# Performance work log

Hardware: AMD Instinct MI355X
Metric: run time of the kernel (lower is better)

Reference implementation:

```python
import jax, jax.numpy as jnp
import numpy as np

N, E, G = 50000, 400000, 500
H, C, IN, ED = 4, 64, 9, 3
NEG = 0.2   # LeakyReLU negative slope (PyG GATv2 default)
EPS = 1e-5  # BatchNorm eps


def _gatv2(x, src, dst, ea, Wl, bl, Wr, We, att, bias):
    # PyG GATv2Conv, concat=False (mean over heads), eval mode (no dropout)
    xl = (x @ Wl + bl).reshape(-1, H, C)   # source transform  [N,H,C]
    xr = (x @ Wr).reshape(-1, H, C)        # target transform  [N,H,C]
    ee = (ea @ We).reshape(-1, H, C)       # edge transform    [E,H,C]
    m = xl[src] + xr[dst] + ee             # [E,H,C]
    s = jnp.einsum('ehc,hc->eh', jax.nn.leaky_relu(m, NEG), att)  # [E,H]
    smax = jax.ops.segment_max(s, dst, num_segments=N)
    ex = jnp.exp(s - smax[dst])
    den = jax.ops.segment_sum(ex, dst, num_segments=N)
    alpha = ex / den[dst]                  # segment softmax over in-edges of dst
    out = jax.ops.segment_sum(xl[src] * alpha[:, :, None], dst, num_segments=N)
    return out.mean(axis=1) + bias         # [N,C]


def _bn(x, g, b, mu, var):
    return (x - mu) * (g * jax.lax.rsqrt(var + EPS)) + b


def setup_inputs() -> dict:
    key = jax.random.key(0)
    ks = jax.random.split(key, 32)
    f = lambda k, s: (jax.random.normal(k, s, jnp.float32) * 0.1)
    inp = dict(
        x=jax.random.normal(ks[0], (N, IN), jnp.float32),
        edge_index=jax.random.randint(ks[1], (2, E), 0, N),
        batch=jnp.sort(jax.random.randint(ks[2], (N,), 0, G)),
        edge_attr=jax.random.normal(ks[3], (E, ED), jnp.float32),
        # input head conv (in=9)
        W0l=f(ks[4], (IN, H * C)), b0l=f(ks[5], (H * C,)),
        W0r=f(ks[6], (IN, H * C)), W0e=f(ks[7], (ED, H * C)),
        a0=f(ks[8], (H, C)), c0=f(ks[9], (C,)),
        # 3 residual conv layers (in=64), stacked
        Wl=f(ks[10], (3, C, H * C)), bl=f(ks[11], (3, H * C)),
        Wr=f(ks[12], (3, C, H * C)), We=f(ks[13], (3, ED, H * C)),
        a=f(ks[14], (3, H, C)), cb=f(ks[15], (3, C)),
        # 4 batchnorms (eval mode running stats)
        bn_g=jnp.ones((4, C), jnp.float32) + f(ks[16], (4, C)),
        bn_b=f(ks[17], (4, C)),
        bn_m=f(ks[18], (4, C)),
        bn_v=jnp.ones((4, C), jnp.float32),
        # output MLP head
        Wo1=f(ks[19], (C, C // 2)), bo1=f(ks[20], (C // 2,)),
        Wo2=f(ks[21], (C // 2, 1)), bo2=f(ks[22], (1,)),
    )
    return inp


def reference(x, edge_index, batch, edge_attr,
              W0l, b0l, W0r, W0e, a0, c0,
              Wl, bl, Wr, We, a, cb,
              bn_g, bn_b, bn_m, bn_v,
              Wo1, bo1, Wo2, bo2):
    src, dst = edge_index[0], edge_index[1]
    h = _gatv2(x, src, dst, edge_attr, W0l, b0l, W0r, W0e, a0, c0)
    h = jax.nn.elu(_bn(h, bn_g[0], bn_b[0], bn_m[0], bn_v[0]))
    for i in range(3):
        z = _gatv2(h, src, dst, edge_attr, Wl[i], bl[i], Wr[i], We[i], a[i], cb[i])
        z = jax.nn.elu(_bn(z, bn_g[i + 1], bn_b[i + 1], bn_m[i + 1], bn_v[i + 1]))
        h = h + z
    # global mean pool over graphs
    cnt = jax.ops.segment_sum(jnp.ones((N,), h.dtype), batch, num_segments=G)
    pooled = jax.ops.segment_sum(h, batch, num_segments=G) / jnp.maximum(cnt, 1.0)[:, None]
    hid = jax.nn.elu(pooled @ Wo1 + bo1)
    return hid @ Wo2 + bo2  # [G,1]
```

## Files before the change

### kernel.cpp

```cpp
#include <hip/hip_runtime.h>
#include <hip/hip_fp16.h>
#include <math.h>

typedef _Float16 h2 __attribute__((ext_vector_type(2)));
typedef _Float16 h8 __attribute__((ext_vector_type(8)));
typedef float f4 __attribute__((ext_vector_type(4)));

#define NWAVES 8192

static __device__ __forceinline__ h2 u2h2(unsigned u) {
    union { unsigned u; h2 h; } x; x.u = u; return x.h;
}

__global__ __launch_bounds__(256) void count_kernel(const int* __restrict__ dst,
                                                    int* __restrict__ deg, int E) {
    int e = blockIdx.x * 256 + threadIdx.x;
    if (e < E) atomicAdd(&deg[dst[e]], 1);
}

#define SCAN_TPB 256
#define SCAN_VPT 4
#define SCAN_ELEMS (SCAN_TPB * SCAN_VPT)

__global__ __launch_bounds__(256) void scan_phase1(const int* __restrict__ deg,
                                                   int* __restrict__ bsum, int n) {
    __shared__ int sh[SCAN_TPB];
    int base = blockIdx.x * SCAN_ELEMS + threadIdx.x * SCAN_VPT;
    int s = 0;
#pragma unroll
    for (int j = 0; j < SCAN_VPT; j++) { int i = base + j; if (i < n) s += deg[i]; }
    sh[threadIdx.x] = s;
    __syncthreads();
    for (int off = 128; off; off >>= 1) {
        if (threadIdx.x < (unsigned)off) sh[threadIdx.x] += sh[threadIdx.x + off];
        __syncthreads();
    }
    if (threadIdx.x == 0) bsum[blockIdx.x] = sh[0];
}

__global__ __launch_bounds__(256) void scan_phase2(int* __restrict__ bsum, int nb,
                                                   int* __restrict__ rowptr, int n) {
    __shared__ int sh[256];
    int v = (threadIdx.x < (unsigned)nb) ? bsum[threadIdx.x] : 0;
    sh[threadIdx.x] = v;
    __syncthreads();
    for (int off = 1; off < 256; off <<= 1) {
        int t = (threadIdx.x >= (unsigned)off) ? sh[threadIdx.x - off] : 0;
        __syncthreads();
        sh[threadIdx.x] += t;
        __syncthreads();
    }
    if (threadIdx.x < (unsigned)nb) bsum[threadIdx.x] = sh[threadIdx.x] - v;
    if (threadIdx.x == 0) rowptr[n] = sh[255];
}

__global__ __launch_bounds__(256) void scan_phase3(const int* __restrict__ deg,
                                                   const int* __restrict__ bsum,
                                                   int* __restrict__ rowptr,
                                                   int* __restrict__ cursor, int n) {
    __shared__ int sh[SCAN_TPB];
    int tid = threadIdx.x;
    int base = blockIdx.x * SCAN_ELEMS + tid * SCAN_VPT;
    int v[SCAN_VPT];
    int s = 0;
#pragma unroll
    for (int j = 0; j < SCAN_VPT; j++) { int i = base + j; v[j] = (i < n) ? deg[i] : 0; s += v[j]; }
    sh[tid] = s;
    __syncthreads();
    for (int off = 1; off < SCAN_TPB; off <<= 1) {
        int t = (tid >= off) ? sh[tid - off] : 0;
        __syncthreads();
        sh[tid] += t;
        __syncthreads();
    }
    int ex = sh[tid] - s + bsum[blockIdx.x];
#pragma unroll
    for (int j = 0; j < SCAN_VPT; j++) {
        int i = base + j;
        if (i < n) { rowptr[i] = ex; cursor[i] = ex; ex += v[j]; }
    }
}

__global__ __launch_bounds__(256) void scatter_kernel(const int* __restrict__ src,
                                                      const int* __restrict__ dst,
                                                      const float* __restrict__ ea,
                                                      int* __restrict__ cursor,
                                                      uint4* __restrict__ csr4, int E) {
    int e = blockIdx.x * 256 + threadIdx.x;
    if (e < E) {
        int d = dst[e];
        int pos = atomicAdd(&cursor[d], 1);
        size_t eb3 = (size_t)e * 3;
        uint4 r;
        r.x = (unsigned)src[e];
        __half2 p0, p1, p2;
        p0.x = p0.y = __float2half_rn(ea[eb3]);
        p1.x = p1.y = __float2half_rn(ea[eb3 + 1]);
        p2.x = p2.y = __float2half_rn(ea[eb3 + 2]);
        r.y = *(unsigned*)&p0; r.z = *(unsigned*)&p1; r.w = *(unsigned*)&p2;
        csr4[pos] = r;
    }
}

__global__ __launch_bounds__(256) void wbal_kernel(const int* __restrict__ rowptr,
                                                   int Nn, int* __restrict__ wstart) {
    int q = blockIdx.x * 256 + threadIdx.x;
    if (q > NWAVES) return;
    if (q == 0) { wstart[0] = 0; return; }
    if (q == NWAVES) { wstart[NWAVES] = Nn; return; }
    int Etot = rowptr[Nn];
    int t = (int)(((long long)q * Etot) / NWAVES);
    int lo = 0, hi = Nn;
    while (lo < hi) {
        int mid = (lo + hi) >> 1;
        if (rowptr[mid] < t) lo = mid + 1; else hi = mid;
    }
    wstart[q] = lo;
}

__global__ __launch_bounds__(256) void bnprep_kernel(const float* __restrict__ c0,
                                                     const float* __restrict__ cb,
                                                     const float* __restrict__ bng,
                                                     const float* __restrict__ bnb,
                                                     const float* __restrict__ bnm,
                                                     const float* __restrict__ bnv,
                                                     float* __restrict__ epi) {
    int t = threadIdx.x;
    int l = t >> 6, c = t & 63;
    float s = bng[l * 64 + c] * rsqrtf(bnv[l * 64 + c] + 1e-5f);
    float bias = (l == 0) ? c0[c] : cb[(l - 1) * 64 + c];
    epi[l * 128 + c] = 0.25f * s;
    epi[l * 128 + 64 + c] = (bias - bnm[l * 64 + c]) * s + bnb[l * 64 + c];
}

__global__ __launch_bounds__(256) void gstart_kernel(const int* __restrict__ batch,
                                                     int* __restrict__ gstart,
                                                     int Nn, int Gg) {
    int n = blockIdx.x * 256 + threadIdx.x;
    if (n >= Nn) return;
    int b = batch[n];
    int prev = (n == 0) ? -1 : batch[n - 1];
    for (int g = prev + 1; g <= b; g++) gstart[g] = n;
    if (n == Nn - 1)
        for (int g = b + 1; g <= Gg; g++) gstart[g] = Nn;
}

__global__ __launch_bounds__(256) void wprep_kernel(const float* __restrict__ W0l,
                                                    const float* __restrict__ W0r,
                                                    const float* __restrict__ Wl,
                                                    const float* __restrict__ Wr,
                                                    __half* __restrict__ Wp) {
    int t = blockIdx.x * 256 + threadIdx.x;
    int layer = t >> 12;
    int r = t & 4095;
    int lane = r & 63;
    int ks = (r >> 6) & 1;
    int gct = r >> 7;
    int K = (layer == 0) ? 9 : 64;
    const float* Wsrc;
    if (layer == 0) Wsrc = (gct < 16) ? W0l : W0r;
    else            Wsrc = ((gct < 16) ? Wl : Wr) + (size_t)(layer - 1) * 64 * 256;
    int cl = ((gct & 15) << 4) + (lane & 15);
    int k0 = (ks << 5) + ((lane >> 4) << 3);
    __half vals[8] __attribute__((aligned(16)));
#pragma unroll
    for (int j = 0; j < 8; j++) {
        int k = k0 + j;
        vals[j] = __float2half_rn((k < K) ? Wsrc[(size_t)k * 256 + cl] : 0.f);
    }
    *(uint4*)(Wp + (size_t)t * 8) = *(const uint4*)vals;
}

template <int K>
__global__ __launch_bounds__(256) void gemm2_mfma_kernel(const float* __restrict__ xin,
                                                         const __half* __restrict__ Wp,
                                                         const float* __restrict__ bl,
                                                         __half* __restrict__ xl,
                                                         __half* __restrict__ xr, int Nn) {
    constexpr int NKS = (K > 32) ? 2 : 1;
    constexpr int KP = NKS * 32;
    __shared__ __align__(16) float shx[32][KP + 4];
    int tid = threadIdx.x;
    int lane = tid & 63;
    int wv = tid >> 6;
    int nb = blockIdx.x * 32;
    int l15 = lane & 15;
    int lg = lane >> 4;

    if (K != KP) {
        for (int q = tid; q < 32 * KP; q += 256) shx[q / KP][q % KP] = 0.f;
        __syncthreads();
    }
    if (K == 64) {
        for (int q = tid; q < 32 * 16; q += 256) {
            int r = q >> 4, c4 = q & 15;
            int node = nb + r;
            float4 v = (node < Nn) ? *(const float4*)(xin + (size_t)node * 64 + c4 * 4)
                                   : make_float4(0.f, 0.f, 0.f, 0.f);
            *(float4*)&shx[r][c4 * 4] = v;
        }
    } else {
        for (int q = tid; q < 32 * K; q += 256) {
            int r = q / K, c = q - r * K;
            int node = nb + r;
            shx[r][c] = (node < Nn) ? xin[(size_t)node * K + c] : 0.f;
        }
    }
    __syncthreads();

    h8 afr[8][NKS];
#pragma unroll
    for (int i = 0; i < 8; i++) {
        int gct = wv * 8 + i;
#pragma unroll
        for (int ks = 0; ks < NKS; ks++)
            afr[i][ks] = *(const h8*)(Wp + (((size_t)(gct * 2 + ks)) * 64 + lane) * 8);
    }
    h8 bfr[2][NKS];
#pragma unroll
    for (int nt = 0; nt < 2; nt++) {
        int row = nt * 16 + l15;
#pragma unroll
        for (int ks = 0; ks < NKS; ks++) {
            int k0 = ks * 32 + lg * 8;
            float4 f0 = *(const float4*)&shx[row][k0];
            float4 f1 = *(const float4*)&shx[row][k0 + 4];
            h8 b;
            b[0] = (_Float16)f0.x; b[1] = (_Float16)f0.y;
            b[2] = (_Float16)f0.z; b[3] = (_Float16)f0.w;
            b[4] = (_Float16)f1.x; b[5] = (_Float16)f1.y;
            b[6] = (_Float16)f1.z; b[7] = (_Float16)f1.w;
            bfr[nt][ks] = b;
        }
    }
    f4 acc[8][2];
#pragma unroll
    for (int i = 0; i < 8; i++) {
        int gct = wv * 8 + i;
        f4 ini;
        if (gct < 16) {
            float4 b4 = *(const float4*)(bl + (gct << 4) + (lg << 2));
            ini[0] = b4.x; ini[1] = b4.y; ini[2] = b4.z; ini[3] = b4.w;
        } else {
            ini[0] = 0.f; ini[1] = 0.f; ini[2] = 0.f; ini[3] = 0.f;
        }
        acc[i][0] = ini;
        acc[i][1] = ini;
    }
#pragma unroll
    for (int i = 0; i < 8; i++)
#pragma unroll
        for (int nt = 0; nt < 2; nt++)
#pragma unroll
            for (int ks = 0; ks < NKS; ks++)
                acc[i][nt] = __builtin_amdgcn_mfma_f32_16x16x32_f16(
                    afr[i][ks], bfr[nt][ks], acc[i][nt], 0, 0, 0);
#pragma unroll
    for (int i = 0; i < 8; i++) {
        int gct = wv * 8 + i;
        __half* outp = (gct < 16) ? xl : xr;
        int cl = ((gct & 15) << 4) + (lg << 2);
#pragma unroll
        for (int nt = 0; nt < 2; nt++) {
            int node = nb + nt * 16 + l15;
            if (node < Nn) {
                __half h4[4] __attribute__((aligned(8)));
                h4[0] = __float2half_rn(acc[i][nt][0]);
                h4[1] = __float2half_rn(acc[i][nt][1]);
                h4[2] = __float2half_rn(acc[i][nt][2]);
                h4[3] = __float2half_rn(acc[i][nt][3]);
                *(uint2*)(outp + (size_t)node * 256 + cl) = *(const uint2*)h4;
            }
        }
    }
}

#define EB 6

#define GISSUE(S, ibase)                                                               \
    {                                                                                  \
        _Pragma("unroll") for (int j = 0; j < EB; j++) {                               \
            int idx = (ibase) + j;                                                     \
            if (idx < end) {                                                           \
                uint4 ce = csr4[idx];                   \
                cey##S[j] = ce.y; cez##S[j] = ce.z; cew##S[j] = ce.w;                  \
                int sn = (int)ce.x;                                                    \
                xpk##S[j] = *(const uint2*)(xl + ((size_t)sn << 8) + (lane << 2));     \
            } else {                                                                   \
                cey##S[j] = 0u; cez##S[j] = 0u; cew##S[j] = 0u;                        \
                xpk##S[j] = make_uint2(0u, 0u);                                        \
            }                                                                          \
        }                                                                              \
    }

#define GCOMPUTE(S, ibase)                                                             \
    {                                                                                  \
        float p[EB];                                                                   \
        _Pragma("unroll") for (int j = 0; j < EB; j++) {                               \
            int idx = (ibase) + j;                                                     \
            if (idx < end) {                                                           \
                h2 ea0 = u2h2(cey##S[j]);                                              \
                h2 ea1 = u2h2(cez##S[j]);                                              \
                h2 ea2 = u2h2(cew##S[j]);                                              \
                h2 xl01 = u2h2(xpk##S[j].x);                                           \
                h2 xl23 = u2h2(xpk##S[j].y);                                           \
                h2 t01 = __builtin_elementwise_fma(ea0, we0a,                          \
                           __builtin_elementwise_fma(ea1, we1a,                        \
                             __builtin_elementwise_fma(ea2, we2a, xr01))) + xl01;      \
                h2 t23 = __builtin_elementwise_fma(ea0, we0b,                          \
                           __builtin_elementwise_fma(ea1, we1b,                        \
                             __builtin_elementwise_fma(ea2, we2b, xr23))) + xl23;      \
                h2 l01 = __builtin_elementwise_max(t01, t01 * c02);                    \
                h2 l23 = __builtin_elementwise_max(t23, t23 * c02);                    \
                p[j] = __builtin_amdgcn_fdot2(l01, atta,                               \
                           __builtin_amdgcn_fdot2(l23, attb, 0.f, false), false);      \
            } else p[j] = -INFINITY;                                                   \
        }                                                                              \
        _Pragma("unroll") for (int off = 1; off < 16; off <<= 1) {                     \
            _Pragma("unroll") for (int j = 0; j < EB; j++) p[j] += __shfl_xor(p[j], off); \
        }                                                                              \
        _Pragma("unroll") for (int j = 0; j < EB; j++) {                               \
            float wv2 = __expf(p[j]);                                                  \
            float2 f0 = __half22float2(*(const __half2*)&xpk##S[j].x);                 \
            float2 f1 = __half22float2(*(const __half2*)&xpk##S[j].y);                 \
            f4 xf; xf[0] = f0.x; xf[1] = f0.y; xf[2] = f1.x; xf[3] = f1.y;             \
            acc = acc + wv2 * xf;                                                      \
            l_run += wv2;                                                              \
        }                                                                              \
    }

__global__ __launch_bounds__(256) void gat_kernel(const __half* __restrict__ xl,
                                                  const __half* __restrict__ xr,
                                                  const float* __restrict__ We,
                                                  const float* __restrict__ att,
                                                  const float* __restrict__ epi,
                                                  const int* __restrict__ rowptr,
                                                  const int* __restrict__ wstart,
                                                  const uint4* __restrict__ csr4,
                                                  float* __restrict__ hout,
                                                  const float* __restrict__ hres,
                                                  int Nn) {
    int tid = threadIdx.x;
    int lane = tid & 63;
    int w = __builtin_amdgcn_readfirstlane(tid >> 6);
    int wave = blockIdx.x * 4 + w;

    float4 we0f = *(const float4*)&We[lane * 4];
    float4 we1f = *(const float4*)&We[256 + lane * 4];
    float4 we2f = *(const float4*)&We[512 + lane * 4];
    float4 attf = *(const float4*)&att[lane * 4];
    h2 we0a = { (_Float16)we0f.x, (_Float16)we0f.y };
    h2 we0b = { (_Float16)we0f.z, (_Float16)we0f.w };
    h2 we1a = { (_Float16)we1f.x, (_Float16)we1f.y };
    h2 we1b = { (_Float16)we1f.z, (_Float16)we1f.w };
    h2 we2a = { (_Float16)we2f.x, (_Float16)we2f.y };
    h2 we2b = { (_Float16)we2f.z, (_Float16)we2f.w };
    h2 atta = { (_Float16)attf.x, (_Float16)attf.y };
    h2 attb = { (_Float16)attf.z, (_Float16)attf.w };
    h2 c02 = { (_Float16)0.2f, (_Float16)0.2f };
    float4 eA = *(const float4*)&epi[(lane & 15) * 4];
    float4 eB4 = *(const float4*)&epi[64 + (lane & 15) * 4];

    int ns = wstart[wave], ne = wstart[wave + 1];
    int d = ns;
    if (d >= ne) return;
    int beg = rowptr[d];
    int end = rowptr[d + 1];
    uint2 xrp = *(const uint2*)(xr + ((size_t)d << 8) + (lane << 2));

    uint2 xpkA[EB], xpkB[EB];
    unsigned ceyA[EB], cezA[EB], cewA[EB], ceyB[EB], cezB[EB], cewB[EB];

    while (d < ne) {
        int dn = d + 1;
        int begn = 0, endn = 0;
        uint2 xrpn = make_uint2(0u, 0u);
        if (dn < ne) {
            begn = rowptr[dn];
            endn = rowptr[dn + 1];
            xrpn = *(const uint2*)(xr + ((size_t)dn << 8) + (lane << 2));
        }
        h2 xr01 = u2h2(xrp.x);
        h2 xr23 = u2h2(xrp.y);

        float l_run = 0.f;
        f4 acc; acc[0] = 0.f; acc[1] = 0.f; acc[2] = 0.f; acc[3] = 0.f;

        int i = beg;
        if (i < end) {
            GISSUE(A, i);
            for (;;) {
                int nx = i + EB;
                if (nx < end) GISSUE(B, nx);
                GCOMPUTE(A, i);
                i = nx;
                if (i >= end) break;
                nx = i + EB;
                if (nx < end) GISSUE(A, nx);
                GCOMPUTE(B, i);
                i = nx;
                if (i >= end) break;
            }
        }
        float inv = (end > beg) ? 1.f / l_run : 0.f;
        float4 o = make_float4(acc[0] * inv, acc[1] * inv, acc[2] * inv, acc[3] * inv);
#pragma unroll
        for (int off = 16; off < 64; off <<= 1) {
            o.x += __shfl_xor(o.x, off);
            o.y += __shfl_xor(o.y, off);
            o.z += __shfl_xor(o.z, off);
            o.w += __shfl_xor(o.w, off);
        }
        if (lane < 16) {
            float vx = fmaf(o.x, eA.x, eB4.x);
            float vy = fmaf(o.y, eA.y, eB4.y);
            float vz = fmaf(o.z, eA.z, eB4.z);
            float vw = fmaf(o.w, eA.w, eB4.w);
            vx = vx > 0.f ? vx : expm1f(vx);
            vy = vy > 0.f ? vy : expm1f(vy);
            vz = vz > 0.f ? vz : expm1f(vz);
            vw = vw > 0.f ? vw : expm1f(vw);
            if (hres) {
                float4 r4 = *(const float4*)&hres[((size_t)d << 6) + (lane << 2)];
                vx += r4.x; vy += r4.y; vz += r4.z; vw += r4.w;
            }
            *(float4*)&hout[((size_t)d << 6) + (lane << 2)] = make_float4(vx, vy, vz, vw);
        }
        d = dn; beg = begn; end = endn; xrp = xrpn;
    }
}

__global__ __launch_bounds__(256) void pool_kernel(const float* __restrict__ h,
                                                   const int* __restrict__ gstart,
                                                   float* __restrict__ pooled, int Gg) {
    __shared__ float red[4][64];
    int g = blockIdx.x;
    int tid = threadIdx.x;
    int lane = tid & 63, w = tid >> 6;
    int gs = gstart[g], ge = gstart[g + 1];
    float s = 0.f;
    for (int n = gs + w; n < ge; n += 4) s += h[((size_t)n << 6) + lane];
    red[w][lane] = s;
    __syncthreads();
    if (tid < 64) {
        float tot = red[0][tid] + red[1][tid] + red[2][tid] + red[3][tid];
        float c = fmaxf((float)(ge - gs), 1.f);
        pooled[((size_t)g << 6) + tid] = tot / c;
    }
}

__global__ __launch_bounds__(64) void head_kernel(const float* __restrict__ pooled,
                                                  const float* __restrict__ Wo1,
                                                  const float* __restrict__ bo1,
                                                  const float* __restrict__ Wo2,
                                                  const float* __restrict__ bo2,
                                                  float* __restrict__ out, int Gg) {
    int g = blockIdx.x;
    int t = threadIdx.x;
    __shared__ float sp[64];
    sp[t] = pooled[(size_t)g * 64 + t];
    __syncthreads();
    float hid = 0.f;
    if (t < 32) {
        hid = bo1[t];
        for (int k = 0; k < 64; k++) hid += sp[k] * Wo1[k * 32 + t];
        hid = hid > 0.f ? hid : expm1f(hid);
        hid *= Wo2[t];
    }
#pragma unroll
    for (int off = 32; off; off >>= 1) hid += __shfl_xor(hid, off);
    if (t == 0) out[g] = hid + bo2[0];
}

extern "C" void kernel_launch(void* const* d_in, const int* in_sizes, int n_in,
                              void* d_out, int out_size, void* d_ws, size_t ws_size,
                              hipStream_t stream) {
    const float* x   = (const float*)d_in[0];
    const int*   ei  = (const int*)d_in[1];
    const int*   bat = (const int*)d_in[2];
    const float* ea  = (const float*)d_in[3];
    const float* W0l = (const float*)d_in[4];
    const float* b0l = (const float*)d_in[5];
    const float* W0r = (const float*)d_in[6];
    const float* W0e = (const float*)d_in[7];
    const float* a0  = (const float*)d_in[8];
    const float* c0  = (const float*)d_in[9];
    const float* Wl  = (const float*)d_in[10];
    const float* bl  = (const float*)d_in[11];
    const float* Wr  = (const float*)d_in[12];
    const float* We  = (const float*)d_in[13];
    const float* a   = (const float*)d_in[14];
    const float* cb  = (const float*)d_in[15];
    const float* bng = (const float*)d_in[16];
    const float* bnb = (const float*)d_in[17];
    const float* bnm = (const float*)d_in[18];
    const float* bnv = (const float*)d_in[19];
    const float* Wo1 = (const float*)d_in[20];
    const float* bo1 = (const float*)d_in[21];
    const float* Wo2 = (const float*)d_in[22];
    const float* bo2 = (const float*)d_in[23];

    int Nn = in_sizes[2];
    int Ee = in_sizes[1] / 2;
    int Gg = out_size;
    const int* srcv = ei;
    const int* dstv = ei + Ee;

    char* w = (char*)d_ws;
    auto alloc = [&](size_t bytes) {
        char* p = w;
        w += (bytes + 255) & ~(size_t)255;
        return p;
    };
    __half* xlb    = (__half*)alloc((size_t)Nn * 256 * 2);
    __half* xrb    = (__half*)alloc((size_t)Nn * 256 * 2);
    float*  hbuf   = (float*)alloc((size_t)Nn * 64 * 4);
    int*    deg    = (int*)alloc((size_t)Nn * 4);
    int*    rowptr = (int*)alloc((size_t)(Nn + 1) * 4);
    int*    cursor = (int*)alloc((size_t)Nn * 4);
    uint4*  csr4   = (uint4*)alloc((size_t)(Ee + 64) * 16);
    float*  pooled = (float*)alloc((size_t)Gg * 64 * 4);
    int*    gstart = (int*)alloc((size_t)(Gg + 1) * 4);
    int*    wstart = (int*)alloc((size_t)(NWAVES + 1) * 4);
    int*    bsum   = (int*)alloc(256 * 4);
    float*  epi    = (float*)alloc(4 * 128 * 4);
    __half* Wp     = (__half*)alloc((size_t)4 * 32768 * 2);

    int nscan = (Nn + SCAN_ELEMS - 1) / SCAN_ELEMS;

    hipMemsetAsync(deg, 0, (size_t)Nn * 4, stream);
    count_kernel<<<(Ee + 255) / 256, 256, 0, stream>>>(dstv, deg, Ee);
    scan_phase1<<<nscan, 256, 0, stream>>>(deg, bsum, Nn);
    scan_phase2<<<1, 256, 0, stream>>>(bsum, nscan, rowptr, Nn);
    scan_phase3<<<nscan, 256, 0, stream>>>(deg, bsum, rowptr, cursor, Nn);
    scatter_kernel<<<(Ee + 255) / 256, 256, 0, stream>>>(srcv, dstv, ea, cursor, csr4, Ee);
    wbal_kernel<<<(NWAVES + 256) / 256, 256, 0, stream>>>(rowptr, Nn, wstart);
    bnprep_kernel<<<1, 256, 0, stream>>>(c0, cb, bng, bnb, bnm, bnv, epi);
    wprep_kernel<<<64, 256, 0, stream>>>(W0l, W0r, Wl, Wr, Wp);
    gstart_kernel<<<(Nn + 255) / 256, 256, 0, stream>>>(bat, gstart, Nn, Gg);

    int gatg = NWAVES / 4;
    int gemg = (Nn + 31) / 32;

    gemm2_mfma_kernel<9><<<gemg, 256, 0, stream>>>(x, Wp, b0l, xlb, xrb, Nn);
    gat_kernel<<<gatg, 256, 0, stream>>>(xlb, xrb, W0e, a0, epi,
                                         rowptr, wstart, csr4, hbuf, nullptr, Nn);
    for (int i = 0; i < 3; i++) {
        gemm2_mfma_kernel<64><<<gemg, 256, 0, stream>>>(
            hbuf, Wp + (size_t)(i + 1) * 32768, bl + (size_t)i * 256, xlb, xrb, Nn);
        gat_kernel<<<gatg, 256, 0, stream>>>(
            xlb, xrb, We + (size_t)i * 768, a + (size_t)i * 256, epi + (size_t)(i + 1) * 128,
            rowptr, wstart, csr4, hbuf, hbuf, Nn);
    }

    pool_kernel<<<Gg, 256, 0, stream>>>(hbuf, gstart, pooled, Gg);
    head_kernel<<<Gg, 64, 0, stream>>>(pooled, Wo1, bo1, Wo2, bo2, (float*)d_out, Gg);
}
```

Baseline: 405.1 us.

## Prefetch next node's first edge batch across nodes and fuse pool with head

The GAT edge loop now keeps a software pipeline that runs across destination-node boundaries. When a node's last batch is being computed, the first batch of the next node's edges and source features is already being loaded, which hides gather latency at every node switch. Separately, the pooling and MLP head kernels are merged into one kernel so the pooled buffer round trip and one launch disappear. The cross-node double buffering adds buffer-parity state and may raise register pressure.

```diff
diff --git a/kernel.cpp b/kernel.cpp
--- a/kernel.cpp
+++ b/kernel.cpp
@@ -277,11 +277,11 @@
 
 #define EB 6
 
-#define GISSUE(S, ibase)                                                               \
+#define GISSUE(S, ibase, iend)                                                         \
     {                                                                                  \
         _Pragma("unroll") for (int j = 0; j < EB; j++) {                               \
             int idx = (ibase) + j;                                                     \
-            if (idx < end) {                                                           \
+            if (idx < (iend)) {                                                        \
                 uint4 ce = csr4[idx];                   \
                 cey##S[j] = ce.y; cez##S[j] = ce.z; cew##S[j] = ce.w;                  \
                 int sn = (int)ce.x;                                                    \
@@ -293,12 +293,12 @@
         }                                                                              \
     }
 
-#define GCOMPUTE(S, ibase)                                                             \
+#define GCOMPUTE(S, ibase, iend)                                                       \
     {                                                                                  \
         float p[EB];                                                                   \
         _Pragma("unroll") for (int j = 0; j < EB; j++) {                               \
             int idx = (ibase) + j;                                                     \
-            if (idx < end) {                                                           \
+            if (idx < (iend)) {                                                        \
                 h2 ea0 = u2h2(cey##S[j]);                                              \
                 h2 ea1 = u2h2(cez##S[j]);                                              \
                 h2 ea2 = u2h2(cew##S[j]);                                              \
@@ -371,6 +371,9 @@
     uint2 xpkA[EB], xpkB[EB];
     unsigned ceyA[EB], cezA[EB], cewA[EB], ceyB[EB], cezB[EB], cewB[EB];
 
+    GISSUE(A, beg, end);
+    int curA = 1;
+
     while (d < ne) {
         int dn = d + 1;
         int begn = 0, endn = 0;
@@ -386,21 +389,24 @@
         float l_run = 0.f;
         f4 acc; acc[0] = 0.f; acc[1] = 0.f; acc[2] = 0.f; acc[3] = 0.f;
 
+        int cnt = end - beg;
+        int nb = (cnt + EB - 1) / EB;
+        if (nb == 0) nb = 1;
         int i = beg;
-        if (i < end) {
-            GISSUE(A, i);
-            for (;;) {
-                int nx = i + EB;
-                if (nx < end) GISSUE(B, nx);
-                GCOMPUTE(A, i);
-                i = nx;
-                if (i >= end) break;
-                nx = i + EB;
-                if (nx < end) GISSUE(A, nx);
-                GCOMPUTE(B, i);
-                i = nx;
-                if (i >= end) break;
+        for (int k = 0; k < nb; k++) {
+            int nxt = i + EB;
+            int ibase, iend;
+            if (nxt < end) { ibase = nxt; iend = end; }
+            else           { ibase = begn; iend = endn; }
+            if (curA) {
+                GISSUE(B, ibase, iend);
+                GCOMPUTE(A, i, end);
+            } else {
+                GISSUE(A, ibase, iend);
+                GCOMPUTE(B, i, end);
             }
+            curA ^= 1;
+            i = nxt;
         }
         float inv = (end > beg) ? 1.f / l_run : 0.f;
         float4 o = make_float4(acc[0] * inv, acc[1] * inv, acc[2] * inv, acc[3] * inv);
@@ -430,10 +436,15 @@
     }
 }
 
-__global__ __launch_bounds__(256) void pool_kernel(const float* __restrict__ h,
-                                                   const int* __restrict__ gstart,
-                                                   float* __restrict__ pooled, int Gg) {
+__global__ __launch_bounds__(256) void poolhead_kernel(const float* __restrict__ h,
+                                                       const int* __restrict__ gstart,
+                                                       const float* __restrict__ Wo1,
+                                                       const float* __restrict__ bo1,
+                                                       const float* __restrict__ Wo2,
+                                                       const float* __restrict__ bo2,
+                                                       float* __restrict__ out, int Gg) {
     __shared__ float red[4][64];
+    __shared__ float sp[64];
     int g = blockIdx.x;
     int tid = threadIdx.x;
     int lane = tid & 63, w = tid >> 6;
@@ -445,31 +456,21 @@
     if (tid < 64) {
         float tot = red[0][tid] + red[1][tid] + red[2][tid] + red[3][tid];
         float c = fmaxf((float)(ge - gs), 1.f);
-        pooled[((size_t)g << 6) + tid] = tot / c;
-    }
-}
-
-__global__ __launch_bounds__(64) void head_kernel(const float* __restrict__ pooled,
-                                                  const float* __restrict__ Wo1,
-                                                  const float* __restrict__ bo1,
-                                                  const float* __restrict__ Wo2,
-                                                  const float* __restrict__ bo2,
-                                                  float* __restrict__ out, int Gg) {
-    int g = blockIdx.x;
-    int t = threadIdx.x;
-    __shared__ float sp[64];
-    sp[t] = pooled[(size_t)g * 64 + t];
+        sp[tid] = tot / c;
+    }
     __syncthreads();
-    float hid = 0.f;
-    if (t < 32) {
-        hid = bo1[t];
-        for (int k = 0; k < 64; k++) hid += sp[k] * Wo1[k * 32 + t];
-        hid = hid > 0.f ? hid : expm1f(hid);
-        hid *= Wo2[t];
-    }
-#pragma unroll
-    for (int off = 32; off; off >>= 1) hid += __shfl_xor(hid, off);
-    if (t == 0) out[g] = hid + bo2[0];
+    if (tid < 64) {
+        float hid = 0.f;
+        if (tid < 32) {
+            hid = bo1[tid];
+            for (int k = 0; k < 64; k++) hid += sp[k] * Wo1[k * 32 + tid];
+            hid = hid > 0.f ? hid : expm1f(hid);
+            hid *= Wo2[tid];
+        }
+#pragma unroll
+        for (int off = 32; off; off >>= 1) hid += __shfl_xor(hid, off);
+        if (tid == 0) out[g] = hid + bo2[0];
+    }
 }
 
 extern "C" void kernel_launch(void* const* d_in, const int* in_sizes, int n_in,
@@ -519,7 +520,6 @@
     int*    rowptr = (int*)alloc((size_t)(Nn + 1) * 4);
     int*    cursor = (int*)alloc((size_t)Nn * 4);
     uint4*  csr4   = (uint4*)alloc((size_t)(Ee + 64) * 16);
-    float*  pooled = (float*)alloc((size_t)Gg * 64 * 4);
     int*    gstart = (int*)alloc((size_t)(Gg + 1) * 4);
     int*    wstart = (int*)alloc((size_t)(NWAVES + 1) * 4);
     int*    bsum   = (int*)alloc(256 * 4);
@@ -553,6 +553,6 @@
             rowptr, wstart, csr4, hbuf, hbuf, Nn);
     }
 
-    pool_kernel<<<Gg, 256, 0, stream>>>(hbuf, gstart, pooled, Gg);
-    head_kernel<<<Gg, 64, 0, stream>>>(pooled, Wo1, bo1, Wo2, bo2, (float*)d_out, Gg);
-}
+    poolhead_kernel<<<Gg, 256, 0, stream>>>(hbuf, gstart, Wo1, bo1, Wo2, bo2,
+                                            (float*)d_out, Gg);
+}
```

After: 434.2 us. 7.2% more time.
